# Optimization experiments

Hardware: AMD Instinct MI355X
Metric: run time of the kernel (lower is better)

The kernel has to match this reference:

```python
import jax, jax.numpy as jnp
import numpy as np

N_QUBITS = 3
MAX_LAYERS = 15
Q_DEPTH = 2


def _apply_ry(state, theta, axis):
    """Apply RY(theta) to qubit `axis` (axes 1..3 of state [B,2,2,2]).
    theta: scalar (shared weight) or [B] (per-sample angle). RY is real.
    """
    st = jnp.moveaxis(state, axis, 1)
    s0, s1 = st[:, 0], st[:, 1]  # [B,2,2]
    c = jnp.cos(theta / 2)
    s = jnp.sin(theta / 2)
    c = c.reshape(c.shape + (1,) * (s0.ndim - c.ndim))
    s = s.reshape(s.shape + (1,) * (s0.ndim - s.ndim))
    new = jnp.stack([c * s0 - s * s1, s * s0 + c * s1], axis=1)
    return jnp.moveaxis(new, 1, axis)


def _cnot(state, ctrl_ax, tgt_ax):
    """CNOT with control/target given as state axes (1..3): flip target where control=1."""
    st = jnp.moveaxis(state, (ctrl_ax, tgt_ax), (1, 2))
    new = jnp.stack([st[:, 0], st[:, 1, ::-1]], axis=1)
    return jnp.moveaxis(new, (1, 2), (ctrl_ax, tgt_ax))


def _quantum_circuit(q_in, q_params):
    """Batched simulation of the PennyLane q_net: H layer, RY(q_in),
    then q_depth x [entangle(CNOT(0,1),CNOT(1,2)); RY(q_weights[k+1])].
    Returns <Z_j> for j=0..2, shape [B, 3]. All gates are real-valued."""
    B = q_in.shape[0]
    qw = q_params.reshape(MAX_LAYERS, N_QUBITS)
    # Hadamards on |000> -> uniform real superposition
    state = jnp.full((B, 2, 2, 2), 1.0 / np.sqrt(8.0), dtype=q_in.dtype)
    for j in range(N_QUBITS):
        state = _apply_ry(state, q_in[:, j], j + 1)
    for k in range(Q_DEPTH):
        state = _cnot(state, 1, 2)  # CNOT(wires=[0,1])
        state = _cnot(state, 2, 3)  # CNOT(wires=[1,2])
        for j in range(N_QUBITS):
            state = _apply_ry(state, qw[k + 1, j], j + 1)
    p = state * state  # probabilities (real amplitudes)
    signs = jnp.array([1.0, -1.0], dtype=p.dtype)
    z = [jnp.sum(jnp.moveaxis(p, j + 1, 1) * signs[None, :, None, None], axis=(1, 2, 3))
         for j in range(N_QUBITS)]
    return jnp.stack(z, axis=-1)  # [B, 3]


def setup_inputs() -> dict:
    key = jax.random.key(0)
    ks = jax.random.split(key, 6)
    B, F, NQ, NOUT = 65536, 512, N_QUBITS, 100
    return {
        "input_features": jax.random.normal(ks[0], (B, F), dtype=jnp.float32),
        "pre_W": jax.random.normal(ks[1], (NQ, F), dtype=jnp.float32) * 0.04,
        "pre_b": jax.random.normal(ks[2], (NQ,), dtype=jnp.float32) * 0.04,
        "q_params": 0.01 * jax.random.normal(ks[3], (MAX_LAYERS * NQ,), dtype=jnp.float32),
        "post_W": jax.random.normal(ks[4], (NOUT, NQ), dtype=jnp.float32) * 0.5,
        "post_b": jax.random.normal(ks[5], (NOUT,), dtype=jnp.float32) * 0.5,
    }


def reference(input_features, pre_W, pre_b, q_params, post_W, post_b):
    pre_out = input_features @ pre_W.T + pre_b          # [B, 3]
    q_in = jnp.tanh(pre_out) * (np.pi / 2.0)             # [B, 3]
    q_out = _quantum_circuit(q_in, q_params)             # [B, 3]
    return q_out @ post_W.T + post_b                     # [B, 100]
```

## Files before the change

### kernel.cpp

```cpp
#include <hip/hip_runtime.h>
#include <math.h>

#define FDIM 512
#define TILE 16
#define WPB  4
#define SPB  (TILE * WPB)

#define RYPAIR(x, y, c, s) { float n0_ = (c)*(x) - (s)*(y); float n1_ = (s)*(x) + (c)*(y); (x) = n0_; (y) = n1_; }
#define SWAPF(x, y) { float t_ = (x); (x) = (y); (y) = t_; }

__global__ __launch_bounds__(256) void qnet_fused(
    const float4* __restrict__ in4,
    const float*  __restrict__ preW,
    const float*  __restrict__ preb,
    const float*  __restrict__ qp,
    const float*  __restrict__ postW,
    const float*  __restrict__ postb,
    float2*       __restrict__ out,
    int B)
{
    __shared__ float Wlds[3 * FDIM];
    __shared__ float pre_lds[WPB][TILE][3];

    const int tid  = threadIdx.x;
    const int lane = tid & 63;
    const int wave = tid >> 6;

    #pragma unroll
    for (int r = 0; r < 6; ++r) Wlds[tid + 256 * r] = preW[tid + 256 * r];
    __syncthreads();

    const float pb0 = preb[0], pb1 = preb[1], pb2 = preb[2];

    float cw[2][3], sw[2][3];
    #pragma unroll
    for (int k = 0; k < 2; ++k)
        #pragma unroll
        for (int j = 0; j < 3; ++j) {
            float th = 0.5f * qp[(k + 1) * 3 + j];
            sw[k][j] = sinf(th);
            cw[k][j] = cosf(th);
        }

    const int ol = (lane < 50) ? lane : 49;
    const float* pw = postW + 6 * ol;
    const float w00 = pw[0], w01 = pw[1], w02 = pw[2];
    const float w10 = pw[3], w11 = pw[4], w12 = pw[5];
    const float b0 = postb[2 * ol], b1 = postb[2 * ol + 1];

    const int tile_base = blockIdx.x * SPB + wave * TILE;
    const int g  = lane >> 3;
    const int kp = lane & 7;

    #pragma unroll
    for (int p = 0; p < 2; ++p) {
        int row = tile_base + 8 * p + g;
        if (row >= B) row = B - 1;
        const float4* rp = in4 + (size_t)row * 128 + kp;
        float4 buf[16];
        #pragma unroll
        for (int i = 0; i < 16; ++i) buf[i] = rp[8 * i];

        float a0a = 0.f, a0b = 0.f, a1a = 0.f, a1b = 0.f, a2a = 0.f, a2b = 0.f;
        #pragma unroll
        for (int i = 0; i < 8; ++i) {
            float4 v0 = buf[2 * i], v1 = buf[2 * i + 1];
            int fb0 = 4 * kp + 64 * i;
            const float4* w0a = (const float4*)(Wlds + fb0);
            const float4* w0b = (const float4*)(Wlds + fb0 + 32);
            const float4* w1a = (const float4*)(Wlds + FDIM + fb0);
            const float4* w1b = (const float4*)(Wlds + FDIM + fb0 + 32);
            const float4* w2a = (const float4*)(Wlds + 2 * FDIM + fb0);
            const float4* w2b = (const float4*)(Wlds + 2 * FDIM + fb0 + 32);
            float4 wa;
            wa = *w0a; a0a = fmaf(v0.w, wa.w, fmaf(v0.z, wa.z, fmaf(v0.y, wa.y, fmaf(v0.x, wa.x, a0a))));
            wa = *w0b; a0b = fmaf(v1.w, wa.w, fmaf(v1.z, wa.z, fmaf(v1.y, wa.y, fmaf(v1.x, wa.x, a0b))));
            wa = *w1a; a1a = fmaf(v0.w, wa.w, fmaf(v0.z, wa.z, fmaf(v0.y, wa.y, fmaf(v0.x, wa.x, a1a))));
            wa = *w1b; a1b = fmaf(v1.w, wa.w, fmaf(v1.z, wa.z, fmaf(v1.y, wa.y, fmaf(v1.x, wa.x, a1b))));
            wa = *w2a; a2a = fmaf(v0.w, wa.w, fmaf(v0.z, wa.z, fmaf(v0.y, wa.y, fmaf(v0.x, wa.x, a2a))));
            wa = *w2b; a2b = fmaf(v1.w, wa.w, fmaf(v1.z, wa.z, fmaf(v1.y, wa.y, fmaf(v1.x, wa.x, a2b))));
        }
        float acc0 = a0a + a0b, acc1 = a1a + a1b, acc2 = a2a + a2b;
        acc0 += __shfl_xor(acc0, 1); acc0 += __shfl_xor(acc0, 2); acc0 += __shfl_xor(acc0, 4);
        acc1 += __shfl_xor(acc1, 1); acc1 += __shfl_xor(acc1, 2); acc1 += __shfl_xor(acc1, 4);
        acc2 += __shfl_xor(acc2, 1); acc2 += __shfl_xor(acc2, 2); acc2 += __shfl_xor(acc2, 4);
        if (kp == 0) {
            int s = 8 * p + g;
            pre_lds[wave][s][0] = acc0;
            pre_lds[wave][s][1] = acc1;
            pre_lds[wave][s][2] = acc2;
        }
    }
    __syncthreads();

    const int myS = lane & 15;
    float d0 = pre_lds[wave][myS][0] + pb0;
    float d1 = pre_lds[wave][myS][1] + pb1;
    float d2 = pre_lds[wave][myS][2] + pb2;

    float t0 = tanhf(d0) * 0.785398163397448f;
    float t1 = tanhf(d1) * 0.785398163397448f;
    float t2 = tanhf(d2) * 0.785398163397448f;
    float s0 = sinf(t0), c0 = cosf(t0);
    float s1 = sinf(t1), c1 = cosf(t1);
    float s2 = sinf(t2), c2 = cosf(t2);

    const float r8 = 0.353553390593274f;
    float u0m = c0 - s0, u0p = c0 + s0;
    float u1m = c1 - s1, u1p = c1 + s1;
    float u2m = (c2 - s2) * r8, u2p = (c2 + s2) * r8;
    float t00 = u0m * u1m, t01 = u0m * u1p, t10 = u0p * u1m, t11 = u0p * u1p;
    float q0 = t00 * u2m, q1 = t00 * u2p;
    float q2 = t01 * u2m, q3 = t01 * u2p;
    float q4 = t10 * u2m, q5 = t10 * u2p;
    float q6 = t11 * u2m, q7 = t11 * u2p;

    #pragma unroll
    for (int k = 0; k < 2; ++k) {
        SWAPF(q4, q6); SWAPF(q5, q7);
        SWAPF(q2, q3); SWAPF(q6, q7);
        float c = cw[k][0], s = sw[k][0];
        RYPAIR(q0, q4, c, s); RYPAIR(q1, q5, c, s); RYPAIR(q2, q6, c, s); RYPAIR(q3, q7, c, s);
        c = cw[k][1]; s = sw[k][1];
        RYPAIR(q0, q2, c, s); RYPAIR(q1, q3, c, s); RYPAIR(q4, q6, c, s); RYPAIR(q5, q7, c, s);
        c = cw[k][2]; s = sw[k][2];
        RYPAIR(q0, q1, c, s); RYPAIR(q2, q3, c, s); RYPAIR(q4, q5, c, s); RYPAIR(q6, q7, c, s);
    }

    float p0 = q0 * q0, p1 = q1 * q1, p2 = q2 * q2, p3 = q3 * q3;
    float p4 = q4 * q4, p5 = q5 * q5, p6 = q6 * q6, p7 = q7 * q7;
    float s01 = p0 + p1, s23 = p2 + p3, s45 = p4 + p5, s67 = p6 + p7;
    float z0 = (s01 + s23) - (s45 + s67);
    float z1 = (s01 - s23) + (s45 - s67);
    float z2 = (p0 - p1) + ((p2 - p3) + ((p4 - p5) + (p6 - p7)));

    #pragma unroll
    for (int s = 0; s < TILE; ++s) {
        float zz0 = __shfl(z0, s);
        float zz1 = __shfl(z1, s);
        float zz2 = __shfl(z2, s);
        int row = tile_base + s;
        float v0 = fmaf(zz2, w02, fmaf(zz1, w01, fmaf(zz0, w00, b0)));
        float v1 = fmaf(zz2, w12, fmaf(zz1, w11, fmaf(zz0, w10, b1)));
        if (lane < 50 && row < B) {
            float2 st; st.x = v0; st.y = v1;
            out[(size_t)row * 50 + lane] = st;
        }
    }
}

extern "C" void kernel_launch(void* const* d_in, const int* in_sizes, int n_in,
                              void* d_out, int out_size, void* d_ws, size_t ws_size,
                              hipStream_t stream) {
    const float4* in4   = (const float4*)d_in[0];
    const float*  preW  = (const float*)d_in[1];
    const float*  preb  = (const float*)d_in[2];
    const float*  qp    = (const float*)d_in[3];
    const float*  postW = (const float*)d_in[4];
    const float*  postb = (const float*)d_in[5];
    float2*       out   = (float2*)d_out;

    int B = in_sizes[0] / FDIM;
    int nblocks = (B + SPB - 1) / SPB;
    qnet_fused<<<nblocks, 256, 0, stream>>>(in4, preW, preb, qp, postW, postb, out, B);
}
```

Measured before the change: 212.1 us.

## Keep pre-projection weights in registers and reduce each row across the full wave

Each lane now holds its slice of the 3x512 pre-weight matrix in registers instead of staging it in LDS, which removes the LDS fill, the block barriers and the per-iteration LDS reads. Each wave processes 8 rows, one row at a time. All 64 lanes load a row and reduce the partial sums with a 6-step wave-wide butterfly. The tile shrinks from 16 to 8 rows per wave, so twice as many blocks are launched and each block reloads the weights and recomputes the sin/cos setup. The full-wave shuffle reduction adds many more cross-lane operations per row, and fewer loads are in flight per lane compared with the earlier 16-deep buffer.

```diff
diff --git a/kernel.cpp b/kernel.cpp
--- a/kernel.cpp
+++ b/kernel.cpp
@@ -2,16 +2,16 @@
 #include <math.h>
 
 #define FDIM 512
-#define TILE 16
+#define TILE 8
 #define WPB  4
 #define SPB  (TILE * WPB)
 
 #define RYPAIR(x, y, c, s) { float n0_ = (c)*(x) - (s)*(y); float n1_ = (s)*(x) + (c)*(y); (x) = n0_; (y) = n1_; }
 #define SWAPF(x, y) { float t_ = (x); (x) = (y); (y) = t_; }
 
-__global__ __launch_bounds__(256) void qnet_fused(
+__global__ __launch_bounds__(256) void qnet_v2(
     const float4* __restrict__ in4,
-    const float*  __restrict__ preW,
+    const float4* __restrict__ preW4,
     const float*  __restrict__ preb,
     const float*  __restrict__ qp,
     const float*  __restrict__ postW,
@@ -19,16 +19,13 @@
     float2*       __restrict__ out,
     int B)
 {
-    __shared__ float Wlds[3 * FDIM];
-    __shared__ float pre_lds[WPB][TILE][3];
-
     const int tid  = threadIdx.x;
     const int lane = tid & 63;
     const int wave = tid >> 6;
 
-    #pragma unroll
-    for (int r = 0; r < 6; ++r) Wlds[tid + 256 * r] = preW[tid + 256 * r];
-    __syncthreads();
+    const float4 w0a = preW4[lane],       w0b = preW4[64 + lane];
+    const float4 w1a = preW4[128 + lane], w1b = preW4[192 + lane];
+    const float4 w2a = preW4[256 + lane], w2b = preW4[320 + lane];
 
     const float pb0 = preb[0], pb1 = preb[1], pb2 = preb[2];
 
@@ -49,54 +46,38 @@
     const float b0 = postb[2 * ol], b1 = postb[2 * ol + 1];
 
     const int tile_base = blockIdx.x * SPB + wave * TILE;
-    const int g  = lane >> 3;
-    const int kp = lane & 7;
 
+    float r0 = 0.f, r1 = 0.f, r2 = 0.f;
     #pragma unroll
-    for (int p = 0; p < 2; ++p) {
-        int row = tile_base + 8 * p + g;
+    for (int s = 0; s < TILE; ++s) {
+        int row = tile_base + s;
         if (row >= B) row = B - 1;
-        const float4* rp = in4 + (size_t)row * 128 + kp;
-        float4 buf[16];
+        const float4* rp = in4 + (size_t)row * 128;
+        float4 i0 = rp[lane];
+        float4 i1 = rp[64 + lane];
+
+        float a0 = fmaf(i0.w, w0a.w, fmaf(i0.z, w0a.z, fmaf(i0.y, w0a.y, i0.x * w0a.x)));
+        a0 = fmaf(i1.w, w0b.w, fmaf(i1.z, w0b.z, fmaf(i1.y, w0b.y, fmaf(i1.x, w0b.x, a0))));
+        float a1 = fmaf(i0.w, w1a.w, fmaf(i0.z, w1a.z, fmaf(i0.y, w1a.y, i0.x * w1a.x)));
+        a1 = fmaf(i1.w, w1b.w, fmaf(i1.z, w1b.z, fmaf(i1.y, w1b.y, fmaf(i1.x, w1b.x, a1))));
+        float a2 = fmaf(i0.w, w2a.w, fmaf(i0.z, w2a.z, fmaf(i0.y, w2a.y, i0.x * w2a.x)));
+        a2 = fmaf(i1.w, w2b.w, fmaf(i1.z, w2b.z, fmaf(i1.y, w2b.y, fmaf(i1.x, w2b.x, a2))));
+
         #pragma unroll
-        for (int i = 0; i < 16; ++i) buf[i] = rp[8 * i];
+        for (int m = 1; m < 64; m <<= 1) {
+            a0 += __shfl_xor(a0, m);
+            a1 += __shfl_xor(a1, m);
+            a2 += __shfl_xor(a2, m);
+        }
+        bool mine = (lane == s);
+        r0 = mine ? a0 : r0;
+        r1 = mine ? a1 : r1;
+        r2 = mine ? a2 : r2;
+    }
 
-        float a0a = 0.f, a0b = 0.f, a1a = 0.f, a1b = 0.f, a2a = 0.f, a2b = 0.f;
-        #pragma unroll
-        for (int i = 0; i < 8; ++i) {
-            float4 v0 = buf[2 * i], v1 = buf[2 * i + 1];
-            int fb0 = 4 * kp + 64 * i;
-            const float4* w0a = (const float4*)(Wlds + fb0);
-            const float4* w0b = (const float4*)(Wlds + fb0 + 32);
-            const float4* w1a = (const float4*)(Wlds + FDIM + fb0);
-            const float4* w1b = (const float4*)(Wlds + FDIM + fb0 + 32);
-            const float4* w2a = (const float4*)(Wlds + 2 * FDIM + fb0);
-            const float4* w2b = (const float4*)(Wlds + 2 * FDIM + fb0 + 32);
-            float4 wa;
-            wa = *w0a; a0a = fmaf(v0.w, wa.w, fmaf(v0.z, wa.z, fmaf(v0.y, wa.y, fmaf(v0.x, wa.x, a0a))));
-            wa = *w0b; a0b = fmaf(v1.w, wa.w, fmaf(v1.z, wa.z, fmaf(v1.y, wa.y, fmaf(v1.x, wa.x, a0b))));
-            wa = *w1a; a1a = fmaf(v0.w, wa.w, fmaf(v0.z, wa.z, fmaf(v0.y, wa.y, fmaf(v0.x, wa.x, a1a))));
-            wa = *w1b; a1b = fmaf(v1.w, wa.w, fmaf(v1.z, wa.z, fmaf(v1.y, wa.y, fmaf(v1.x, wa.x, a1b))));
-            wa = *w2a; a2a = fmaf(v0.w, wa.w, fmaf(v0.z, wa.z, fmaf(v0.y, wa.y, fmaf(v0.x, wa.x, a2a))));
-            wa = *w2b; a2b = fmaf(v1.w, wa.w, fmaf(v1.z, wa.z, fmaf(v1.y, wa.y, fmaf(v1.x, wa.x, a2b))));
-        }
-        float acc0 = a0a + a0b, acc1 = a1a + a1b, acc2 = a2a + a2b;
-        acc0 += __shfl_xor(acc0, 1); acc0 += __shfl_xor(acc0, 2); acc0 += __shfl_xor(acc0, 4);
-        acc1 += __shfl_xor(acc1, 1); acc1 += __shfl_xor(acc1, 2); acc1 += __shfl_xor(acc1, 4);
-        acc2 += __shfl_xor(acc2, 1); acc2 += __shfl_xor(acc2, 2); acc2 += __shfl_xor(acc2, 4);
-        if (kp == 0) {
-            int s = 8 * p + g;
-            pre_lds[wave][s][0] = acc0;
-            pre_lds[wave][s][1] = acc1;
-            pre_lds[wave][s][2] = acc2;
-        }
-    }
-    __syncthreads();
-
-    const int myS = lane & 15;
-    float d0 = pre_lds[wave][myS][0] + pb0;
-    float d1 = pre_lds[wave][myS][1] + pb1;
-    float d2 = pre_lds[wave][myS][2] + pb2;
+    float d0 = r0 + pb0;
+    float d1 = r1 + pb1;
+    float d2 = r2 + pb2;
 
     float t0 = tanhf(d0) * 0.785398163397448f;
     float t1 = tanhf(d1) * 0.785398163397448f;
@@ -153,7 +134,7 @@
                               void* d_out, int out_size, void* d_ws, size_t ws_size,
                               hipStream_t stream) {
     const float4* in4   = (const float4*)d_in[0];
-    const float*  preW  = (const float*)d_in[1];
+    const float4* preW4 = (const float4*)d_in[1];
     const float*  preb  = (const float*)d_in[2];
     const float*  qp    = (const float*)d_in[3];
     const float*  postW = (const float*)d_in[4];
@@ -162,5 +143,5 @@
 
     int B = in_sizes[0] / FDIM;
     int nblocks = (B + SPB - 1) / SPB;
-    qnet_fused<<<nblocks, 256, 0, stream>>>(in4, preW, preb, qp, postW, postb, out, B);
+    qnet_v2<<<nblocks, 256, 0, stream>>>(in4, preW4, preb, qp, postW, postb, out, B);
 }
```

After: 208.2 us. Within noise of the previous version (-1.8%).
